# Optimization experiments

Hardware: AMD Instinct MI355X
Metric: run time of the kernel (lower is better)

The kernel has to match this reference:

```python
import jax, jax.numpy as jnp
import numpy as np

N_NODES = 50000
N_EDGES = 800000


def setup_inputs() -> dict:
    key = jax.random.key(0)
    k1, k2, k3, k4 = jax.random.split(key, 4)
    x = jax.random.normal(k1, (N_NODES, 128), dtype=jnp.float32)
    edge_index = jax.random.randint(k2, (2, N_EDGES), 0, N_NODES, dtype=jnp.int64)
    W1 = jax.random.normal(k3, (128, 64), dtype=jnp.float32) / np.sqrt(128.0)
    b1 = jnp.zeros((64,), dtype=jnp.float32)
    W2 = jax.random.normal(k4, (64, 40), dtype=jnp.float32) / np.sqrt(64.0)
    b2 = jnp.zeros((40,), dtype=jnp.float32)
    return {"x": x, "edge_index": edge_index, "W1": W1, "b1": b1, "W2": W2, "b2": b2}


def _gcn_norm(edge_index, n_nodes):
    # Add self-loops, then compute symmetric normalization D^{-1/2} A D^{-1/2}
    loop = jnp.arange(n_nodes, dtype=edge_index.dtype)
    row = jnp.concatenate([edge_index[0], loop])  # source
    col = jnp.concatenate([edge_index[1], loop])  # target
    ones = jnp.ones(row.shape[0], dtype=jnp.float32)
    deg = jax.ops.segment_sum(ones, col, num_segments=n_nodes)
    dinv = jnp.where(deg > 0, jax.lax.rsqrt(deg), 0.0)
    norm = dinv[row] * dinv[col]  # [E + N]
    return row, col, norm


def _gcn_conv(h, W, b, row, col, norm, n_nodes):
    hw = h @ W                         # transform first (smaller messages)
    msg = hw[row] * norm[:, None]      # gather + scale per edge
    agg = jax.ops.segment_sum(msg, col, num_segments=n_nodes)
    return agg + b


def reference(x, edge_index, W1, b1, W2, b2):
    n = x.shape[0]
    row, col, norm = _gcn_norm(edge_index, n)
    h = _gcn_conv(x, W1, b1, row, col, norm, n)
    h = jax.nn.relu(h)
    h = _gcn_conv(h, W2, b2, row, col, norm, n)
    return jax.nn.softmax(h, axis=-1)
```

## Files before the change

kernel.cpp:

```cpp
#include <hip/hip_runtime.h>

#define N_NODES 50000
#define N_EDGES 800000
#define F_IN   128
#define F_MID  64
#define F_OUT  40

#define SLICE_SHIFT 8
#define SLICE_SZ    256
#define NSLICE      196
#define PCHUNKS     256
#define PCHUNK_E    ((N_EDGES + PCHUNKS - 1) / PCHUNKS)
#define NCOUNT      (NSLICE * PCHUNKS)



__global__ __launch_bounds__(256) void bucket_count(const int* __restrict__ ei,
                                                    int* __restrict__ counts) {
    __shared__ int cnt[NSLICE];
    if (threadIdx.x < NSLICE) cnt[threadIdx.x] = 0;
    __syncthreads();
    int e0 = blockIdx.x * PCHUNK_E;
    int e1 = e0 + PCHUNK_E; if (e1 > N_EDGES) e1 = N_EDGES;
    for (int e = e0 + threadIdx.x; e < e1; e += 256) {
        int c = ei[N_EDGES + e];
        atomicAdd(&cnt[c >> SLICE_SHIFT], 1);
    }
    __syncthreads();
    if (threadIdx.x < NSLICE) counts[threadIdx.x * PCHUNKS + blockIdx.x] = cnt[threadIdx.x];
}


__global__ __launch_bounds__(256) void sc_bsum(const int* __restrict__ counts, int* __restrict__ bsum) {
    int idx = blockIdx.x * 256 + threadIdx.x;
    int v = (idx < NCOUNT) ? counts[idx] : 0;
#pragma unroll
    for (int off = 32; off > 0; off >>= 1) v += __shfl_xor(v, off, 64);
    __shared__ int ws[4];
    if ((threadIdx.x & 63) == 0) ws[threadIdx.x >> 6] = v;
    __syncthreads();
    if (threadIdx.x == 0) bsum[blockIdx.x] = ws[0] + ws[1] + ws[2] + ws[3];
}

__global__ __launch_bounds__(256) void sc_bscan(const int* __restrict__ bsum, int* __restrict__ boff) {
    int tid = threadIdx.x;
    int lane = tid & 63, wv = tid >> 6;
    int v = (tid < NSLICE) ? bsum[tid] : 0;
    int inc = v;
#pragma unroll
    for (int s = 1; s < 64; s <<= 1) {
        int t = __shfl_up(inc, s, 64);
        if (lane >= s) inc += t;
    }
    __shared__ int ws[4];
    if (lane == 63) ws[wv] = inc;
    __syncthreads();
    int woff = 0;
    for (int w = 0; w < wv; ++w) woff += ws[w];
    if (tid < NSLICE) boff[tid] = woff + inc - v;
}

__global__ __launch_bounds__(256) void sc_bscan2(const int* __restrict__ counts,
                                                 const int* __restrict__ boff,
                                                 int* __restrict__ choff) {
    int idx = blockIdx.x * 256 + threadIdx.x;
    int lane = threadIdx.x & 63, wv = threadIdx.x >> 6;
    int v = (idx < NCOUNT) ? counts[idx] : 0;
    int inc = v;
#pragma unroll
    for (int s = 1; s < 64; s <<= 1) {
        int t = __shfl_up(inc, s, 64);
        if (lane >= s) inc += t;
    }
    __shared__ int ws[4];
    if (lane == 63) ws[wv] = inc;
    __syncthreads();
    int off = boff[blockIdx.x];
    for (int w = 0; w < wv; ++w) off += ws[w];
    if (idx < NCOUNT) choff[idx] = off + inc - v;
}


__global__ __launch_bounds__(256) void bucket_scatter(const int* __restrict__ ei,
                                                      const int* __restrict__ choff,
                                                      int* __restrict__ pairs) {
    __shared__ int cur[NSLICE];
    if (threadIdx.x < NSLICE) cur[threadIdx.x] = choff[threadIdx.x * PCHUNKS + blockIdx.x];
    __syncthreads();
    int e0 = blockIdx.x * PCHUNK_E;
    int e1 = e0 + PCHUNK_E; if (e1 > N_EDGES) e1 = N_EDGES;
    for (int e = e0 + threadIdx.x; e < e1; e += 256) {
        int r = ei[e];
        int c = ei[N_EDGES + e];
        int pos = atomicAdd(&cur[c >> SLICE_SHIFT], 1);
        pairs[pos] = r | ((c & (SLICE_SZ - 1)) << 16);
    }
}


__global__ __launch_bounds__(256) void slice_csr(const int* __restrict__ pairs,
                                                 const int* __restrict__ choff,
                                                 int* __restrict__ rowptr,
                                                 float* __restrict__ dinv,
                                                 int* __restrict__ srcs) {
    __shared__ int hist[SLICE_SZ];
    __shared__ int wpart[4];
    int s = blockIdx.x;
    int base = choff[s * PCHUNKS];
    int end  = (s == NSLICE - 1) ? N_EDGES : choff[(s + 1) * PCHUNKS];
    int tid = threadIdx.x;
    hist[tid] = 0;
    __syncthreads();
    for (int i = base + tid; i < end; i += 256)
        atomicAdd(&hist[pairs[i] >> 16], 1);
    __syncthreads();
    int v = hist[tid];
    int lane = tid & 63, wv = tid >> 6;
    int inc = v;
#pragma unroll
    for (int st = 1; st < 64; st <<= 1) {
        int t = __shfl_up(inc, st, 64);
        if (lane >= st) inc += t;
    }
    if (lane == 63) wpart[wv] = inc;
    __syncthreads();
    int woff = 0;
    for (int w = 0; w < wv; ++w) woff += wpart[w];
    int ex = woff + inc - v;
    __syncthreads();
    hist[tid] = ex;
    int node = s * SLICE_SZ + tid;
    if (node < N_NODES) {
        rowptr[node] = base + ex;
        dinv[node]   = rsqrtf((float)v + 1.0f);
    }
    if (node == N_NODES - 1) rowptr[N_NODES] = N_EDGES;
    __syncthreads();
    for (int i = base + tid; i < end; i += 256) {
        int p = pairs[i];
        int pos = atomicAdd(&hist[p >> 16], 1);
        srcs[base + pos] = p & 0xFFFF;
    }
}


__global__ __launch_bounds__(256) void gemm1_kernel(const float* __restrict__ x,
                                                    const float* __restrict__ W1,
                                                    const float* __restrict__ dinv,
                                                    float* __restrict__ hw1s) {
    __shared__ float sW[F_IN * F_MID];
    __shared__ float sX[64][68];
    int tid = threadIdx.x;
    const float4* W4 = (const float4*)W1;
    float4* sW4 = (float4*)sW;
    for (int i = tid; i < F_IN * F_MID / 4; i += 256) sW4[i] = W4[i];

    int row0 = blockIdx.x * 64;
    int tx = tid & 15, ty = tid >> 4;
    int c0 = tx * 4, r0 = ty * 4;
    float acc[4][4] = {};

    for (int p = 0; p < 2; ++p) {
        __syncthreads();
#pragma unroll
        for (int it = 0; it < 4; ++it) {
            int i = (tid + it * 256) * 4;
            int r = i >> 6, k = i & 63;
            float4 v = make_float4(0.f, 0.f, 0.f, 0.f);
            if (row0 + r < N_NODES)
                v = *(const float4*)&x[(size_t)(row0 + r) * F_IN + p * 64 + k];
            *(float4*)&sX[r][k] = v;
        }
        __syncthreads();
        const float* sWp = sW + p * 64 * F_MID;
#pragma unroll 4
        for (int k = 0; k < 64; ++k) {
            float4 w = *(const float4*)&sWp[k * F_MID + c0];
            float a0 = sX[r0 + 0][k];
            float a1 = sX[r0 + 1][k];
            float a2 = sX[r0 + 2][k];
            float a3 = sX[r0 + 3][k];
            acc[0][0] = fmaf(a0, w.x, acc[0][0]); acc[0][1] = fmaf(a0, w.y, acc[0][1]);
            acc[0][2] = fmaf(a0, w.z, acc[0][2]); acc[0][3] = fmaf(a0, w.w, acc[0][3]);
            acc[1][0] = fmaf(a1, w.x, acc[1][0]); acc[1][1] = fmaf(a1, w.y, acc[1][1]);
            acc[1][2] = fmaf(a1, w.z, acc[1][2]); acc[1][3] = fmaf(a1, w.w, acc[1][3]);
            acc[2][0] = fmaf(a2, w.x, acc[2][0]); acc[2][1] = fmaf(a2, w.y, acc[2][1]);
            acc[2][2] = fmaf(a2, w.z, acc[2][2]); acc[2][3] = fmaf(a2, w.w, acc[2][3]);
            acc[3][0] = fmaf(a3, w.x, acc[3][0]); acc[3][1] = fmaf(a3, w.y, acc[3][1]);
            acc[3][2] = fmaf(a3, w.z, acc[3][2]); acc[3][3] = fmaf(a3, w.w, acc[3][3]);
        }
    }
#pragma unroll
    for (int j = 0; j < 4; ++j) {
        int row = row0 + r0 + j;
        if (row < N_NODES) {
            float d = dinv[row];
            float4 o = make_float4(acc[j][0] * d, acc[j][1] * d, acc[j][2] * d, acc[j][3] * d);
            *(float4*)&hw1s[(size_t)row * F_MID + c0] = o;
        }
    }
}


__global__ __launch_bounds__(256) void gather1_kernel(const int* __restrict__ rowptr,
                                                      const int* __restrict__ srcs,
                                                      const float* __restrict__ hw1s,
                                                      const float* __restrict__ dinv,
                                                      const float* __restrict__ b1,
                                                      float* __restrict__ h) {
    int n = blockIdx.x * 4 + (threadIdx.x >> 6);
    int lane = threadIdx.x & 63;
    if (n >= N_NODES) return;
    int s = rowptr[n], e = rowptr[n + 1];
    float acc = 0.f;
    for (int base = s; base < e; base += 64) {
        int cnt = e - base; if (cnt > 64) cnt = 64;
        int ms = (lane < cnt) ? srcs[base + lane] : 0;
        int j = 0;
        for (; j + 8 <= cnt; j += 8) {
            int i0 = __shfl(ms, j, 64),     i1 = __shfl(ms, j + 1, 64);
            int i2 = __shfl(ms, j + 2, 64), i3 = __shfl(ms, j + 3, 64);
            int i4 = __shfl(ms, j + 4, 64), i5 = __shfl(ms, j + 5, 64);
            int i6 = __shfl(ms, j + 6, 64), i7 = __shfl(ms, j + 7, 64);
            float v0 = hw1s[(size_t)i0 * F_MID + lane];
            float v1 = hw1s[(size_t)i1 * F_MID + lane];
            float v2 = hw1s[(size_t)i2 * F_MID + lane];
            float v3 = hw1s[(size_t)i3 * F_MID + lane];
            float v4 = hw1s[(size_t)i4 * F_MID + lane];
            float v5 = hw1s[(size_t)i5 * F_MID + lane];
            float v6 = hw1s[(size_t)i6 * F_MID + lane];
            float v7 = hw1s[(size_t)i7 * F_MID + lane];
            acc += ((v0 + v1) + (v2 + v3)) + ((v4 + v5) + (v6 + v7));
        }
        for (; j < cnt; ++j) {
            int i0 = __shfl(ms, j, 64);
            acc += hw1s[(size_t)i0 * F_MID + lane];
        }
    }
    float d = dinv[n];
    float v = fmaf(d, acc + hw1s[(size_t)n * F_MID + lane], b1[lane]);
    h[(size_t)n * F_MID + lane] = fmaxf(v, 0.f);
}


__global__ __launch_bounds__(256) void gemm2_kernel(const float* __restrict__ h,
                                                    const float* __restrict__ W2,
                                                    const float* __restrict__ dinv,
                                                    float* __restrict__ hw2s) {
    __shared__ float sW[F_MID * F_OUT];
    for (int i = threadIdx.x; i < F_MID * F_OUT; i += 256) sW[i] = W2[i];
    __syncthreads();
    int idx = blockIdx.x * 256 + threadIdx.x;
    if (idx >= N_NODES * F_OUT) return;
    int r = idx / F_OUT;
    int c = idx % F_OUT;
    float acc = 0.f;
#pragma unroll
    for (int k = 0; k < F_MID; ++k) acc = fmaf(h[(size_t)r * F_MID + k], sW[k * F_OUT + c], acc);
    hw2s[idx] = acc * dinv[r];
}


__global__ __launch_bounds__(256) void gather2_softmax_kernel(const int* __restrict__ rowptr,
                                                              const int* __restrict__ srcs,
                                                              const float* __restrict__ hw2s,
                                                              const float* __restrict__ dinv,
                                                              const float* __restrict__ b2,
                                                              float* __restrict__ out) {
    int n = blockIdx.x * 4 + (threadIdx.x >> 6);
    int lane = threadIdx.x & 63;
    if (n >= N_NODES) return;
    int s = rowptr[n], e = rowptr[n + 1];
    float acc = 0.f;
    for (int base = s; base < e; base += 64) {
        int cnt = e - base; if (cnt > 64) cnt = 64;
        int ms = (lane < cnt) ? srcs[base + lane] : 0;
        int j = 0;
        for (; j + 8 <= cnt; j += 8) {
            int i0 = __shfl(ms, j, 64),     i1 = __shfl(ms, j + 1, 64);
            int i2 = __shfl(ms, j + 2, 64), i3 = __shfl(ms, j + 3, 64);
            int i4 = __shfl(ms, j + 4, 64), i5 = __shfl(ms, j + 5, 64);
            int i6 = __shfl(ms, j + 6, 64), i7 = __shfl(ms, j + 7, 64);
            if (lane < F_OUT) {
                float v0 = hw2s[(size_t)i0 * F_OUT + lane];
                float v1 = hw2s[(size_t)i1 * F_OUT + lane];
                float v2 = hw2s[(size_t)i2 * F_OUT + lane];
                float v3 = hw2s[(size_t)i3 * F_OUT + lane];
                float v4 = hw2s[(size_t)i4 * F_OUT + lane];
                float v5 = hw2s[(size_t)i5 * F_OUT + lane];
                float v6 = hw2s[(size_t)i6 * F_OUT + lane];
                float v7 = hw2s[(size_t)i7 * F_OUT + lane];
                acc += ((v0 + v1) + (v2 + v3)) + ((v4 + v5) + (v6 + v7));
            }
        }
        for (; j < cnt; ++j) {
            int i0 = __shfl(ms, j, 64);
            if (lane < F_OUT) acc += hw2s[(size_t)i0 * F_OUT + lane];
        }
    }
    float d = dinv[n];
    float v = -3.402823466e38f;
    if (lane < F_OUT)
        v = fmaf(d, acc + hw2s[(size_t)n * F_OUT + lane], b2[lane]);
    float m = v;
#pragma unroll
    for (int off = 32; off > 0; off >>= 1) m = fmaxf(m, __shfl_xor(m, off, 64));
    float p = (lane < F_OUT) ? __expf(v - m) : 0.f;
    float su = p;
#pragma unroll
    for (int off = 32; off > 0; off >>= 1) su += __shfl_xor(su, off, 64);
    if (lane < F_OUT) out[(size_t)n * F_OUT + lane] = p / su;
}


extern "C" void kernel_launch(void* const* d_in, const int* in_sizes, int n_in,
                              void* d_out, int out_size, void* d_ws, size_t ws_size,
                              hipStream_t stream) {
    const float* x  = (const float*)d_in[0];
    const int*   ei = (const int*)d_in[1];
    const float* W1 = (const float*)d_in[2];
    const float* b1 = (const float*)d_in[3];
    const float* W2 = (const float*)d_in[4];
    const float* b2 = (const float*)d_in[5];
    float* out = (float*)d_out;

    char* ws = (char*)d_ws;
    size_t off = 0;
    auto alloc = [&](size_t bytes) -> void* {
        void* p = ws + off;
        off += (bytes + 255) & ~(size_t)255;
        return p;
    };
    int*   counts = (int*)  alloc(NCOUNT * sizeof(int));
    int*   bsum   = (int*)  alloc(NSLICE * sizeof(int));
    int*   boff   = (int*)  alloc(NSLICE * sizeof(int));
    int*   choff  = (int*)  alloc(NCOUNT * sizeof(int));
    int*   pairs  = (int*)  alloc((size_t)N_EDGES * sizeof(int));
    int*   rowptr = (int*)  alloc((N_NODES + 1) * sizeof(int));
    float* dinv   = (float*)alloc(N_NODES * sizeof(float));
    int*   srcs   = (int*)  alloc((size_t)N_EDGES * sizeof(int));
    float* hw1s   = (float*)alloc((size_t)N_NODES * F_MID * sizeof(float));
    float* h      = (float*)alloc((size_t)N_NODES * F_MID * sizeof(float));
    float* hw2s   = (float*)alloc((size_t)N_NODES * F_OUT * sizeof(float));

    bucket_count  <<<PCHUNKS, 256, 0, stream>>>(ei, counts);
    sc_bsum       <<<(NCOUNT + 255) / 256, 256, 0, stream>>>(counts, bsum);
    sc_bscan      <<<1, 256, 0, stream>>>(bsum, boff);
    sc_bscan2     <<<(NCOUNT + 255) / 256, 256, 0, stream>>>(counts, boff, choff);
    bucket_scatter<<<PCHUNKS, 256, 0, stream>>>(ei, choff, pairs);
    slice_csr     <<<NSLICE, 256, 0, stream>>>(pairs, choff, rowptr, dinv, srcs);
    gemm1_kernel  <<<(N_NODES + 63) / 64, 256, 0, stream>>>(x, W1, dinv, hw1s);
    gather1_kernel<<<(N_NODES + 3) / 4, 256, 0, stream>>>(rowptr, srcs, hw1s, dinv, b1, h);
    gemm2_kernel  <<<(N_NODES * F_OUT + 255) / 256, 256, 0, stream>>>(h, W2, dinv, hw2s);
    gather2_softmax_kernel<<<(N_NODES + 3) / 4, 256, 0, stream>>>(rowptr, srcs, hw2s, dinv, b2, out);
}
```

Baseline: 216.8 us.

## Build CSR in one cooperative kernel and fuse gather1 with gemm2

```diff
diff --git a/kernel.cpp b/kernel.cpp
--- a/kernel.cpp
+++ b/kernel.cpp
@@ -1,4 +1,7 @@
 #include <hip/hip_runtime.h>
+#include <hip/hip_cooperative_groups.h>
+
+namespace cg = cooperative_groups;
 
 #define N_NODES 50000
 #define N_EDGES 800000
@@ -6,140 +9,79 @@
 #define F_MID  64
 #define F_OUT  40
 
-#define SLICE_SHIFT 8
-#define SLICE_SZ    256
-#define NSLICE      196
-#define PCHUNKS     256
-#define PCHUNK_E    ((N_EDGES + PCHUNKS - 1) / PCHUNKS)
-#define NCOUNT      (NSLICE * PCHUNKS)
-
-
-
-__global__ __launch_bounds__(256) void bucket_count(const int* __restrict__ ei,
-                                                    int* __restrict__ counts) {
-    __shared__ int cnt[NSLICE];
-    if (threadIdx.x < NSLICE) cnt[threadIdx.x] = 0;
-    __syncthreads();
-    int e0 = blockIdx.x * PCHUNK_E;
-    int e1 = e0 + PCHUNK_E; if (e1 > N_EDGES) e1 = N_EDGES;
-    for (int e = e0 + threadIdx.x; e < e1; e += 256) {
-        int c = ei[N_EDGES + e];
-        atomicAdd(&cnt[c >> SLICE_SHIFT], 1);
-    }
-    __syncthreads();
-    if (threadIdx.x < NSLICE) counts[threadIdx.x * PCHUNKS + blockIdx.x] = cnt[threadIdx.x];
-}
-
-
-__global__ __launch_bounds__(256) void sc_bsum(const int* __restrict__ counts, int* __restrict__ bsum) {
-    int idx = blockIdx.x * 256 + threadIdx.x;
-    int v = (idx < NCOUNT) ? counts[idx] : 0;
-#pragma unroll
-    for (int off = 32; off > 0; off >>= 1) v += __shfl_xor(v, off, 64);
-    __shared__ int ws[4];
-    if ((threadIdx.x & 63) == 0) ws[threadIdx.x >> 6] = v;
-    __syncthreads();
-    if (threadIdx.x == 0) bsum[blockIdx.x] = ws[0] + ws[1] + ws[2] + ws[3];
-}
-
-__global__ __launch_bounds__(256) void sc_bscan(const int* __restrict__ bsum, int* __restrict__ boff) {
-    int tid = threadIdx.x;
-    int lane = tid & 63, wv = tid >> 6;
-    int v = (tid < NSLICE) ? bsum[tid] : 0;
-    int inc = v;
-#pragma unroll
-    for (int s = 1; s < 64; s <<= 1) {
-        int t = __shfl_up(inc, s, 64);
-        if (lane >= s) inc += t;
-    }
-    __shared__ int ws[4];
-    if (lane == 63) ws[wv] = inc;
-    __syncthreads();
-    int woff = 0;
-    for (int w = 0; w < wv; ++w) woff += ws[w];
-    if (tid < NSLICE) boff[tid] = woff + inc - v;
-}
-
-__global__ __launch_bounds__(256) void sc_bscan2(const int* __restrict__ counts,
-                                                 const int* __restrict__ boff,
-                                                 int* __restrict__ choff) {
-    int idx = blockIdx.x * 256 + threadIdx.x;
-    int lane = threadIdx.x & 63, wv = threadIdx.x >> 6;
-    int v = (idx < NCOUNT) ? counts[idx] : 0;
-    int inc = v;
-#pragma unroll
-    for (int s = 1; s < 64; s <<= 1) {
-        int t = __shfl_up(inc, s, 64);
-        if (lane >= s) inc += t;
-    }
-    __shared__ int ws[4];
-    if (lane == 63) ws[wv] = inc;
-    __syncthreads();
-    int off = boff[blockIdx.x];
-    for (int w = 0; w < wv; ++w) off += ws[w];
-    if (idx < NCOUNT) choff[idx] = off + inc - v;
-}
-
-
-__global__ __launch_bounds__(256) void bucket_scatter(const int* __restrict__ ei,
-                                                      const int* __restrict__ choff,
-                                                      int* __restrict__ pairs) {
-    __shared__ int cur[NSLICE];
-    if (threadIdx.x < NSLICE) cur[threadIdx.x] = choff[threadIdx.x * PCHUNKS + blockIdx.x];
-    __syncthreads();
-    int e0 = blockIdx.x * PCHUNK_E;
-    int e1 = e0 + PCHUNK_E; if (e1 > N_EDGES) e1 = N_EDGES;
-    for (int e = e0 + threadIdx.x; e < e1; e += 256) {
+#define NSLICE 196
+#define BUILD_GRID 1024
+
+
+__global__ __launch_bounds__(256, 4) void build_csr(const int* __restrict__ ei,
+                                                    int* __restrict__ deg,
+                                                    int* __restrict__ rowptr,
+                                                    float* __restrict__ dinv,
+                                                    int* __restrict__ cursor,
+                                                    int* __restrict__ srcs,
+                                                    int* __restrict__ bsum) {
+    cg::grid_group grid = cg::this_grid();
+    __shared__ int wpart[4];
+    const int tid  = threadIdx.x;
+    const int gtid = blockIdx.x * 256 + tid;
+    const int gsz  = gridDim.x * 256;
+
+    for (int i = gtid; i < N_NODES; i += gsz) deg[i] = 0;
+    grid.sync();
+
+    for (int e = gtid; e < N_EDGES; e += gsz) atomicAdd(&deg[ei[N_EDGES + e]], 1);
+    grid.sync();
+
+    if (blockIdx.x < NSLICE) {
+        int node = blockIdx.x * 256 + tid;
+        int v = (node < N_NODES) ? deg[node] : 0;
+        int lane = tid & 63, wv = tid >> 6;
+        int inc = v;
+#pragma unroll
+        for (int st = 1; st < 64; st <<= 1) {
+            int t = __shfl_up(inc, st, 64);
+            if (lane >= st) inc += t;
+        }
+        if (lane == 63) wpart[wv] = inc;
+        __syncthreads();
+        int woff = 0;
+        for (int w = 0; w < wv; ++w) woff += wpart[w];
+        if (node < N_NODES) rowptr[node] = woff + inc - v;
+        if (tid == 255) bsum[blockIdx.x] = woff + inc;
+    }
+    grid.sync();
+
+    if (blockIdx.x == 0) {
+        int v = (tid < NSLICE) ? bsum[tid] : 0;
+        int lane = tid & 63, wv = tid >> 6;
+        int inc = v;
+#pragma unroll
+        for (int st = 1; st < 64; st <<= 1) {
+            int t = __shfl_up(inc, st, 64);
+            if (lane >= st) inc += t;
+        }
+        if (lane == 63) wpart[wv] = inc;
+        __syncthreads();
+        int woff = 0;
+        for (int w = 0; w < wv; ++w) woff += wpart[w];
+        if (tid < NSLICE) bsum[tid] = woff + inc - v;
+    }
+    grid.sync();
+
+    for (int n = gtid; n < N_NODES; n += gsz) {
+        int rp = rowptr[n] + bsum[n >> 8];
+        rowptr[n] = rp;
+        cursor[n] = rp;
+        dinv[n]   = rsqrtf((float)deg[n] + 1.0f);
+    }
+    if (gtid == 0) rowptr[N_NODES] = N_EDGES;
+    grid.sync();
+
+    for (int e = gtid; e < N_EDGES; e += gsz) {
         int r = ei[e];
         int c = ei[N_EDGES + e];
-        int pos = atomicAdd(&cur[c >> SLICE_SHIFT], 1);
-        pairs[pos] = r | ((c & (SLICE_SZ - 1)) << 16);
-    }
-}
-
-
-__global__ __launch_bounds__(256) void slice_csr(const int* __restrict__ pairs,
-                                                 const int* __restrict__ choff,
-                                                 int* __restrict__ rowptr,
-                                                 float* __restrict__ dinv,
-                                                 int* __restrict__ srcs) {
-    __shared__ int hist[SLICE_SZ];
-    __shared__ int wpart[4];
-    int s = blockIdx.x;
-    int base = choff[s * PCHUNKS];
-    int end  = (s == NSLICE - 1) ? N_EDGES : choff[(s + 1) * PCHUNKS];
-    int tid = threadIdx.x;
-    hist[tid] = 0;
-    __syncthreads();
-    for (int i = base + tid; i < end; i += 256)
-        atomicAdd(&hist[pairs[i] >> 16], 1);
-    __syncthreads();
-    int v = hist[tid];
-    int lane = tid & 63, wv = tid >> 6;
-    int inc = v;
-#pragma unroll
-    for (int st = 1; st < 64; st <<= 1) {
-        int t = __shfl_up(inc, st, 64);
-        if (lane >= st) inc += t;
-    }
-    if (lane == 63) wpart[wv] = inc;
-    __syncthreads();
-    int woff = 0;
-    for (int w = 0; w < wv; ++w) woff += wpart[w];
-    int ex = woff + inc - v;
-    __syncthreads();
-    hist[tid] = ex;
-    int node = s * SLICE_SZ + tid;
-    if (node < N_NODES) {
-        rowptr[node] = base + ex;
-        dinv[node]   = rsqrtf((float)v + 1.0f);
-    }
-    if (node == N_NODES - 1) rowptr[N_NODES] = N_EDGES;
-    __syncthreads();
-    for (int i = base + tid; i < end; i += 256) {
-        int p = pairs[i];
-        int pos = atomicAdd(&hist[p >> 16], 1);
-        srcs[base + pos] = p & 0xFFFF;
+        int pos = atomicAdd(&cursor[c], 1);
+        srcs[pos] = r;
     }
 }
 
@@ -202,15 +144,18 @@
 }
 
 
-__global__ __launch_bounds__(256) void gather1_kernel(const int* __restrict__ rowptr,
-                                                      const int* __restrict__ srcs,
-                                                      const float* __restrict__ hw1s,
-                                                      const float* __restrict__ dinv,
-                                                      const float* __restrict__ b1,
-                                                      float* __restrict__ h) {
+__global__ __launch_bounds__(256) void gather1_gemm2(const int* __restrict__ rowptr,
+                                                     const int* __restrict__ srcs,
+                                                     const float* __restrict__ hw1s,
+                                                     const float* __restrict__ dinv,
+                                                     const float* __restrict__ b1,
+                                                     const float* __restrict__ W2,
+                                                     float* __restrict__ hw2s) {
+    __shared__ float sW[F_MID * F_OUT];
+    for (int i = threadIdx.x; i < F_MID * F_OUT; i += 256) sW[i] = W2[i];
+    __syncthreads();
     int n = blockIdx.x * 4 + (threadIdx.x >> 6);
     int lane = threadIdx.x & 63;
-    if (n >= N_NODES) return;
     int s = rowptr[n], e = rowptr[n + 1];
     float acc = 0.f;
     for (int base = s; base < e; base += 64) {
@@ -238,26 +183,16 @@
         }
     }
     float d = dinv[n];
-    float v = fmaf(d, acc + hw1s[(size_t)n * F_MID + lane], b1[lane]);
-    h[(size_t)n * F_MID + lane] = fmaxf(v, 0.f);
-}
-
-
-__global__ __launch_bounds__(256) void gemm2_kernel(const float* __restrict__ h,
-                                                    const float* __restrict__ W2,
-                                                    const float* __restrict__ dinv,
-                                                    float* __restrict__ hw2s) {
-    __shared__ float sW[F_MID * F_OUT];
-    for (int i = threadIdx.x; i < F_MID * F_OUT; i += 256) sW[i] = W2[i];
-    __syncthreads();
-    int idx = blockIdx.x * 256 + threadIdx.x;
-    if (idx >= N_NODES * F_OUT) return;
-    int r = idx / F_OUT;
-    int c = idx % F_OUT;
-    float acc = 0.f;
-#pragma unroll
-    for (int k = 0; k < F_MID; ++k) acc = fmaf(h[(size_t)r * F_MID + k], sW[k * F_OUT + c], acc);
-    hw2s[idx] = acc * dinv[r];
+    float hv = fmaxf(fmaf(d, acc + hw1s[(size_t)n * F_MID + lane], b1[lane]), 0.f);
+
+    int cl = (lane < F_OUT) ? lane : 0;
+    float o = 0.f;
+#pragma unroll
+    for (int k = 0; k < F_MID; ++k) {
+        float hk = __shfl(hv, k, 64);
+        o = fmaf(hk, sW[k * F_OUT + cl], o);
+    }
+    if (lane < F_OUT) hw2s[(size_t)n * F_OUT + lane] = o * d;
 }
 
 
@@ -331,26 +266,21 @@
         off += (bytes + 255) & ~(size_t)255;
         return p;
     };
-    int*   counts = (int*)  alloc(NCOUNT * sizeof(int));
-    int*   bsum   = (int*)  alloc(NSLICE * sizeof(int));
-    int*   boff   = (int*)  alloc(NSLICE * sizeof(int));
-    int*   choff  = (int*)  alloc(NCOUNT * sizeof(int));
-    int*   pairs  = (int*)  alloc((size_t)N_EDGES * sizeof(int));
+    int*   deg    = (int*)  alloc(N_NODES * sizeof(int));
     int*   rowptr = (int*)  alloc((N_NODES + 1) * sizeof(int));
     float* dinv   = (float*)alloc(N_NODES * sizeof(float));
+    int*   cursor = (int*)  alloc(N_NODES * sizeof(int));
     int*   srcs   = (int*)  alloc((size_t)N_EDGES * sizeof(int));
+    int*   bsum   = (int*)  alloc(256 * sizeof(int));
     float* hw1s   = (float*)alloc((size_t)N_NODES * F_MID * sizeof(float));
-    float* h      = (float*)alloc((size_t)N_NODES * F_MID * sizeof(float));
     float* hw2s   = (float*)alloc((size_t)N_NODES * F_OUT * sizeof(float));
 
-    bucket_count  <<<PCHUNKS, 256, 0, stream>>>(ei, counts);
-    sc_bsum       <<<(NCOUNT + 255) / 256, 256, 0, stream>>>(counts, bsum);
-    sc_bscan      <<<1, 256, 0, stream>>>(bsum, boff);
-    sc_bscan2     <<<(NCOUNT + 255) / 256, 256, 0, stream>>>(counts, boff, choff);
-    bucket_scatter<<<PCHUNKS, 256, 0, stream>>>(ei, choff, pairs);
-    slice_csr     <<<NSLICE, 256, 0, stream>>>(pairs, choff, rowptr, dinv, srcs);
+    void* args[] = {(void*)&ei, (void*)&deg, (void*)&rowptr, (void*)&dinv,
+                    (void*)&cursor, (void*)&srcs, (void*)&bsum};
+    hipLaunchCooperativeKernel((void*)build_csr, dim3(BUILD_GRID), dim3(256),
+                               args, 0, stream);
+
     gemm1_kernel  <<<(N_NODES + 63) / 64, 256, 0, stream>>>(x, W1, dinv, hw1s);
-    gather1_kernel<<<(N_NODES + 3) / 4, 256, 0, stream>>>(rowptr, srcs, hw1s, dinv, b1, h);
-    gemm2_kernel  <<<(N_NODES * F_OUT + 255) / 256, 256, 0, stream>>>(h, W2, dinv, hw2s);
+    gather1_gemm2 <<<N_NODES / 4, 256, 0, stream>>>(rowptr, srcs, hw1s, dinv, b1, W2, hw2s);
     gather2_softmax_kernel<<<(N_NODES + 3) / 4, 256, 0, stream>>>(rowptr, srcs, hw2s, dinv, b2, out);
 }
```

New measurement: 773.3 us. 257% more time.
